# Performance work log

Hardware: AMD Instinct MI355X
Metric: run time of the kernel (lower is better)

The kernel has to match this reference:

```python
import jax, jax.numpy as jnp
import numpy as np

LEN_EPISODE = 2048
DT = 0.01
B = 16384


def setup_inputs() -> dict:
    key = jax.random.key(0)
    k1, k2 = jax.random.split(key)
    init_conds = jax.random.normal(k1, (B, 2), dtype=jnp.float32)  # (theta, theta_dot)
    # params: omega, gamma, A, phi -- positive, O(1) values
    params = jax.random.uniform(k2, (B, 4), dtype=jnp.float32)
    return {"init_conds": init_conds, "params": params}


def _pendulum_solve(init_conds, params, len_episode=LEN_EPISODE, dt=DT):
    omega = params[:, 0:1]  # (B,1)
    gamma = params[:, 1:2]
    A = params[:, 2:3]
    phi = params[:, 3:4]
    t = jnp.linspace(0.0, dt * (len_episode - 1), len_episode)

    def fun(ti, s):
        # s: (B,2) = [theta, theta_dot]
        th = s[:, 0:1]
        thdot = s[:, 1:2]
        force = A * omega * omega * jnp.cos(2.0 * jnp.pi * phi * ti)
        dth2 = force - gamma * thdot - omega * omega * jnp.sin(th)
        return jnp.concatenate([thdot, dth2], axis=-1)

    def step(y, ti):
        # torchdiffeq fixed-grid 'rk4' uses the 3/8-rule (rk4_alt_step_func)
        k1 = fun(ti, y)
        k2 = fun(ti + dt / 3.0, y + dt * k1 / 3.0)
        k3 = fun(ti + 2.0 * dt / 3.0, y + dt * (k2 - k1 / 3.0))
        k4 = fun(ti + dt, y + dt * (k1 - k2 + k3))
        y_next = y + dt * (k1 + 3.0 * (k2 + k3) + k4) * 0.125
        return y_next, y_next

    _, ys = jax.lax.scan(step, init_conds, t[:-1])
    sol = jnp.concatenate([init_conds[None], ys], axis=0)  # (T, B, 2)
    x = sol[:, :, 0].T  # (B, T): observed angle theta
    return x


def reference(init_conds, params):
    return _pendulum_solve(init_conds, params)
```

## Files before the change

### kernel.cpp

```cpp
#include <hip/hip_runtime.h>

#define LEN_EPISODE 2048
#define TW 6.283185307179586
#define HH 0.16


#define STEPH() do {                                                        \
    const float f1 = Atil * rcf;                                            \
    const float f2 = __builtin_fmaf(nA2s, rsf, A2c * rcf);                  \
    const float f3 = __builtin_fmaf(nA3s, rsf, A3c * rcf);                  \
    rcn = __builtin_fmaf(nsdf, rsf, rcf * cdf);                             \
    rsn = __builtin_fmaf(sdf, rcf, rsf * cdf);                              \
    const float f4 = Atil * rcn;                                            \
    const float s1 = __builtin_amdgcn_sinf(U);                              \
    const float U2 = __builtin_fmaf(c13, V, U);                             \
    const float s2 = __builtin_amdgcn_sinf(U2);                             \
    const float k1w = __builtin_fmaf(nw2t, s1, __builtin_fmaf(ngam, V, f1)); \
    const float V2 = __builtin_fmaf(c13, k1w, V);                           \
    const float k2w = __builtin_fmaf(nw2t, s2, __builtin_fmaf(ngam, V2, f2)); \
    const float U3 = __builtin_fmaf(hh, V2, __builtin_fmaf(nc13, V, U));    \
    const float V3 = __builtin_fmaf(hh, k2w, __builtin_fmaf(nc13, k1w, V)); \
    const float s3 = __builtin_amdgcn_sinf(U3);                             \
    const float k3w = __builtin_fmaf(nw2t, s3, __builtin_fmaf(ngam, V3, f3)); \
    const float U4 = __builtin_fmaf(hh, (V - V2) + V3, U);                  \
    const float V4 = __builtin_fmaf(hh, (k1w - k2w) + k3w, V);              \
    const float s4 = __builtin_amdgcn_sinf(U4);                             \
    const float k4w = __builtin_fmaf(nw2t, s4, __builtin_fmaf(ngam, V4, f4)); \
    Un = __builtin_fmaf(h8, __builtin_fmaf(3.0f, V2 + V3, V) + V4, U);      \
    Vn = __builtin_fmaf(h8, __builtin_fmaf(3.0f, k2w + k3w, k1w) + k4w, V); \
} while (0)

#define B00(t) ((1.0-(t))*(1.0-(t))*(1.0+2.0*(t)))
#define B10(t) ((t)*(1.0-(t))*(1.0-(t)))
#define B01(t) ((t)*(t)*(3.0-2.0*(t)))
#define B11(t) ((t)*(t)*((t)-1.0))
#define HERMT(t)                                                              \
    __builtin_fmaf((float)(TW * B00(t)), U,                                   \
    __builtin_fmaf((float)(TW * B10(t) * HH), V,                              \
    __builtin_fmaf((float)(TW * B01(t)), Un, (float)(TW * B11(t) * HH) * Vn)))

#define EMIT15(dst) do {                                                      \
    (dst)[0]  = HERMT( 1.0/16.0); (dst)[1]  = HERMT( 2.0/16.0);               \
    (dst)[2]  = HERMT( 3.0/16.0); (dst)[3]  = HERMT( 4.0/16.0);               \
    (dst)[4]  = HERMT( 5.0/16.0); (dst)[5]  = HERMT( 6.0/16.0);               \
    (dst)[6]  = HERMT( 7.0/16.0); (dst)[7]  = HERMT( 8.0/16.0);               \
    (dst)[8]  = HERMT( 9.0/16.0); (dst)[9]  = HERMT(10.0/16.0);               \
    (dst)[10] = HERMT(11.0/16.0); (dst)[11] = HERMT(12.0/16.0);               \
    (dst)[12] = HERMT(13.0/16.0); (dst)[13] = HERMT(14.0/16.0);               \
    (dst)[14] = HERMT(15.0/16.0);                                             \
} while (0)

#define COMMIT() do { U = Un; V = Vn; rcf = rcn; rsf = rsn; } while (0)

__global__ __launch_bounds__(512) void pend_kernel(
    const float* __restrict__ init,
    const float* __restrict__ params,
    float* __restrict__ out,
    int B)
{
    __shared__ float lds[8 * 16 * 65];

    const int tid  = threadIdx.x;
    const int lane = tid & 63;
    const int wv   = tid >> 6;
    const int b = blockIdx.x * 64 + lane;
    if (b >= B) return;

    const float2 ic = *reinterpret_cast<const float2*>(init + 2 * b);
    const float4 p  = *reinterpret_cast<const float4*>(params + 4 * b);
    const float omega = p.x, gamma = p.y, A = p.z, phi = p.w;

    const float twopi  = 6.283185307179586f;
    const float inv2pi = 0.15915494309189535f;

    float U = ic.x * inv2pi;
    float V = ic.y * inv2pi;

    const float hh   = 0.16f;
    const float c13  = (float)(0.16 / 3.0);
    const float nc13 = -c13;
    const float h8   = 0.02f;
    const float ngam = -gamma;
    const float nw2t = -(omega * omega) * inv2pi;
    const float Atil = A * omega * omega * inv2pi;

    const double c_d = 6.283185307179586476925287 * (double)phi;
    const float cdf  = (float)::cos(c_d * 0.16);
    const float sdf  = (float)::sin(c_d * 0.16);
    const float nsdf = -sdf;
    const float A2c  = Atil * (float)::cos(c_d * (0.16 / 3.0));
    const float nA2s = -Atil * (float)::sin(c_d * (0.16 / 3.0));
    const float A3c  = Atil * (float)::cos(c_d * (0.32 / 3.0));
    const float nA3s = -Atil * (float)::sin(c_d * (0.32 / 3.0));

    float rcf = 1.0f, rsf = 0.0f;
    float Un, Vn, rcn, rsn;

    const int r16 = lane >> 2;
    const int q2  = lane & 3;
    float* __restrict__ outblk = out + (size_t)(blockIdx.x * 64) * LEN_EPISODE;
    float* __restrict__ ldsw = lds + wv * (16 * 65);

    const int kbeg = wv << 4;

    float va[16];

#pragma unroll 2
    for (int k = 0; k < kbeg; ++k) {
        STEPH(); COMMIT();
    }

    for (int k = kbeg; k < kbeg + 16; ++k) {
        va[0] = (k == 0) ? ic.x : twopi * U;
        STEPH(); EMIT15(va + 1); COMMIT();

#pragma unroll
        for (int j = 0; j < 16; ++j)
            ldsw[j * 65 + lane] = va[j];

        const int colb = k << 4;
#pragma unroll
        for (int rb = 0; rb < 4; ++rb) {
            const int row = (rb << 4) + r16;
            float4 v;
            v.x = ldsw[(4 * q2 + 0) * 65 + row];
            v.y = ldsw[(4 * q2 + 1) * 65 + row];
            v.z = ldsw[(4 * q2 + 2) * 65 + row];
            v.w = ldsw[(4 * q2 + 3) * 65 + row];
            *reinterpret_cast<float4*>(outblk + (size_t)row * LEN_EPISODE + colb + 4 * q2) = v;
        }
    }
}

extern "C" void kernel_launch(void* const* d_in, const int* in_sizes, int n_in,
                              void* d_out, int out_size, void* d_ws, size_t ws_size,
                              hipStream_t stream) {
    const float* init   = (const float*)d_in[0];
    const float* params = (const float*)d_in[1];
    float* out = (float*)d_out;
    const int B = in_sizes[0] / 2;

    const int block = 512;
    const int grid  = B / 64;
    pend_kernel<<<grid, block, 0, stream>>>(init, params, out, B);
}
```

Measured before the change: 34.04 us.

## Split block into one integrator wave and six writer waves via LDS ring

Instead of every wave redundantly re-integrating the prefix up to its chunk, one wave runs all 128 coarse RK steps and publishes states to an LDS ring buffer with a release counter. Six consumer waves spin on the counter, Hermite-interpolate the outputs, transpose through LDS, and store them. This removes redundant prefix integration, which grows with wave index, but serializes the whole time integration onto a single wave. It also adds spin-wait synchronization, and one wave (wv 4) sits idle.

```diff
diff --git a/kernel.cpp b/kernel.cpp
--- a/kernel.cpp
+++ b/kernel.cpp
@@ -58,76 +58,99 @@
     float* __restrict__ out,
     int B)
 {
-    __shared__ float lds[8 * 16 * 65];
+    __shared__ float2 ring[64][64];
+    __shared__ float  stag[6][16 * 65];
+    __shared__ int    cnt;
 
     const int tid  = threadIdx.x;
     const int lane = tid & 63;
     const int wv   = tid >> 6;
     const int b = blockIdx.x * 64 + lane;
-    if (b >= B) return;
-
-    const float2 ic = *reinterpret_cast<const float2*>(init + 2 * b);
-    const float4 p  = *reinterpret_cast<const float4*>(params + 4 * b);
-    const float omega = p.x, gamma = p.y, A = p.z, phi = p.w;
 
     const float twopi  = 6.283185307179586f;
     const float inv2pi = 0.15915494309189535f;
 
-    float U = ic.x * inv2pi;
-    float V = ic.y * inv2pi;
+    const float2 ic = *reinterpret_cast<const float2*>(init + 2 * b);
 
-    const float hh   = 0.16f;
-    const float c13  = (float)(0.16 / 3.0);
-    const float nc13 = -c13;
-    const float h8   = 0.02f;
-    const float ngam = -gamma;
-    const float nw2t = -(omega * omega) * inv2pi;
-    const float Atil = A * omega * omega * inv2pi;
+    if (tid == 0) cnt = 0;
+    __syncthreads();
 
-    const double c_d = 6.283185307179586476925287 * (double)phi;
-    const float cdf  = (float)::cos(c_d * 0.16);
-    const float sdf  = (float)::sin(c_d * 0.16);
-    const float nsdf = -sdf;
-    const float A2c  = Atil * (float)::cos(c_d * (0.16 / 3.0));
-    const float nA2s = -Atil * (float)::sin(c_d * (0.16 / 3.0));
-    const float A3c  = Atil * (float)::cos(c_d * (0.32 / 3.0));
-    const float nA3s = -Atil * (float)::sin(c_d * (0.32 / 3.0));
+    if (wv == 0) {
+        const float4 p  = *reinterpret_cast<const float4*>(params + 4 * b);
+        const float omega = p.x, gamma = p.y, A = p.z, phi = p.w;
 
-    float rcf = 1.0f, rsf = 0.0f;
-    float Un, Vn, rcn, rsn;
+        float U = ic.x * inv2pi;
+        float V = ic.y * inv2pi;
 
-    const int r16 = lane >> 2;
-    const int q2  = lane & 3;
-    float* __restrict__ outblk = out + (size_t)(blockIdx.x * 64) * LEN_EPISODE;
-    float* __restrict__ ldsw = lds + wv * (16 * 65);
+        const float hh   = 0.16f;
+        const float c13  = (float)(0.16 / 3.0);
+        const float nc13 = -c13;
+        const float h8   = 0.02f;
+        const float ngam = -gamma;
+        const float nw2t = -(omega * omega) * inv2pi;
+        const float Atil = A * omega * omega * inv2pi;
 
-    const int kbeg = wv << 4;
+        const double c_d = 6.283185307179586476925287 * (double)phi;
+        const float cdf  = (float)::cos(c_d * 0.16);
+        const float sdf  = (float)::sin(c_d * 0.16);
+        const float nsdf = -sdf;
+        const float A2c  = Atil * (float)::cos(c_d * (0.16 / 3.0));
+        const float nA2s = -Atil * (float)::sin(c_d * (0.16 / 3.0));
+        const float A3c  = Atil * (float)::cos(c_d * (0.32 / 3.0));
+        const float nA3s = -Atil * (float)::sin(c_d * (0.32 / 3.0));
 
-    float va[16];
+        float rcf = 1.0f, rsf = 0.0f;
+        float Un, Vn, rcn, rsn;
 
-#pragma unroll 2
-    for (int k = 0; k < kbeg; ++k) {
-        STEPH(); COMMIT();
-    }
+        for (int k = 0; k < 128; ++k) {
+            ring[k & 63][lane] = make_float2(U, V);
+            __threadfence_block();
+            if (lane == 0)
+                __hip_atomic_store(&cnt, k + 1, __ATOMIC_RELEASE,
+                                   __HIP_MEMORY_SCOPE_WORKGROUP);
+            STEPH(); COMMIT();
+        }
+        ring[128 & 63][lane] = make_float2(U, V);
+        __threadfence_block();
+        if (lane == 0)
+            __hip_atomic_store(&cnt, 129, __ATOMIC_RELEASE,
+                               __HIP_MEMORY_SCOPE_WORKGROUP);
+    } else if (wv != 4) {
+        const int eid = (wv < 4) ? (wv - 1) : (wv - 2);
+        float* __restrict__ stg = &stag[eid][0];
+        const int r16 = lane >> 2;
+        const int q2  = lane & 3;
+        float* __restrict__ outblk = out + (size_t)(blockIdx.x * 64) * LEN_EPISODE;
 
-    for (int k = kbeg; k < kbeg + 16; ++k) {
-        va[0] = (k == 0) ? ic.x : twopi * U;
-        STEPH(); EMIT15(va + 1); COMMIT();
+        float va[16];
+
+        for (int k = eid; k < 128; k += 6) {
+            while (__hip_atomic_load(&cnt, __ATOMIC_ACQUIRE,
+                                     __HIP_MEMORY_SCOPE_WORKGROUP) < k + 2) {
+                __builtin_amdgcn_s_sleep(1);
+            }
+            const float2 s0 = ring[k & 63][lane];
+            const float2 s1 = ring[(k + 1) & 63][lane];
+            const float U = s0.x, V = s0.y, Un = s1.x, Vn = s1.y;
+
+            va[0] = (k == 0) ? ic.x : twopi * U;
+            EMIT15(va + 1);
 
 #pragma unroll
-        for (int j = 0; j < 16; ++j)
-            ldsw[j * 65 + lane] = va[j];
+            for (int j = 0; j < 16; ++j)
+                stg[j * 65 + lane] = va[j];
 
-        const int colb = k << 4;
+            const int colb = k << 4;
 #pragma unroll
-        for (int rb = 0; rb < 4; ++rb) {
-            const int row = (rb << 4) + r16;
-            float4 v;
-            v.x = ldsw[(4 * q2 + 0) * 65 + row];
-            v.y = ldsw[(4 * q2 + 1) * 65 + row];
-            v.z = ldsw[(4 * q2 + 2) * 65 + row];
-            v.w = ldsw[(4 * q2 + 3) * 65 + row];
-            *reinterpret_cast<float4*>(outblk + (size_t)row * LEN_EPISODE + colb + 4 * q2) = v;
+            for (int rb = 0; rb < 4; ++rb) {
+                const int row = (rb << 4) + r16;
+                float4 v;
+                v.x = stg[(4 * q2 + 0) * 65 + row];
+                v.y = stg[(4 * q2 + 1) * 65 + row];
+                v.z = stg[(4 * q2 + 2) * 65 + row];
+                v.w = stg[(4 * q2 + 3) * 65 + row];
+                *reinterpret_cast<float4*>(outblk + (size_t)row * LEN_EPISODE + colb + 4 * q2) = v;
+            }
         }
     }
 }
```

New measurement: 32.17 us. 5.5% less time.
